# Optimization experiments

Measured on AMD Instinct MI355X. Metric: run time of the kernel, lower is better.

## Reference

```python
import jax, jax.numpy as jnp
import numpy as np
from jax import lax

EPS = 1e-5
MIN_SAMPLES = 4
RESHAPE = 14        # edge-map downsample factor
KEEP_FRAC = 0.1     # 1 - quantile(0.9)
KERNEL_FRAC = 0.05  # eval-mode log_kernel

SOBEL_X = jnp.array([[-1., 0., 1.], [-2., 0., 2.], [-1., 0., 1.]], jnp.float32)
SOBEL_Y = jnp.array([[-1., -2., -1.], [0., 0., 0.], [1., 2., 1.]], jnp.float32)


def _dwconv3(x, k):
    C = x.shape[1]
    kern = jnp.broadcast_to(k, (C, 1, 3, 3)).astype(x.dtype)
    return lax.conv_general_dilated(x, kern, (1, 1), 'SAME',
        feature_group_count=C, dimension_numbers=('NCHW', 'OIHW', 'NCHW'))


def _erode3(m):
    k = jnp.ones((1, 1, 3, 3), m.dtype)
    s = lax.conv_general_dilated(m, k, (1, 1), 'SAME',
        dimension_numbers=('NCHW', 'OIHW', 'NCHW'))
    return (s >= 9.0).astype(m.dtype)


def _masked_mean(x, mask, axis=-1):
    m = mask.astype(x.dtype)
    return jnp.sum(x * m, axis=axis) / jnp.maximum(jnp.sum(m, axis=axis), 1.0)


def _ssi_norm(x, mask):
    # scale-shift-invariant normalization: masked median shift, masked MAD scale
    big = jnp.where(mask, x, jnp.inf)
    srt = jnp.sort(big, axis=-1)
    n = jnp.sum(mask, axis=-1)
    idx = jnp.maximum((n - 1) // 2, 0)
    med = jnp.take_along_axis(srt, idx[..., None], axis=-1)
    med = jnp.where(n[..., None] > 0, med, 0.0)
    scale = _masked_mean(jnp.abs(x - med), mask, axis=-1)[..., None]
    return (x - med) / jnp.maximum(scale, EPS)


def _get_edge(image, vmask):
    gx = _dwconv3(image, SOBEL_X) / 8.0
    gy = _dwconv3(image, SOBEL_Y) / 8.0
    gx = jnp.sqrt(jnp.mean(gx * gx, axis=1, keepdims=True))
    gy = jnp.sqrt(jnp.mean(gy * gy, axis=1, keepdims=True))
    edges = jnp.sqrt(gx * gx + gy * gy)
    H, W = edges.shape[-2:]
    bm = jnp.zeros((H, W), edges.dtype).at[3:H - 3, 3:W - 3].set(1.0)
    return edges * bm * vmask


def _resize_bilinear(x, oh, ow):
    # torch F.interpolate bilinear, align_corners=False, no antialias
    B, C, H, W = x.shape
    def coords(o, s):
        c = jnp.clip((jnp.arange(o) + 0.5) * (s / o) - 0.5, 0.0, s - 1.0)
        i0 = jnp.floor(c).astype(jnp.int32)
        return i0, jnp.minimum(i0 + 1, s - 1), c - i0
    y0, y1, wy = coords(oh, H)
    x0, x1, wx = coords(ow, W)
    wy = wy[:, None]; wx = wx[None, :]
    g = lambda yi, xi: x[:, :, yi[:, None], xi[None, :]]
    return (g(y0, x0) * (1 - wy) * (1 - wx) + g(y0, x1) * (1 - wy) * wx
          + g(y1, x0) * wy * (1 - wx) + g(y1, x1) * wy * wx)


def _sample_edges(edges):
    B, _, H, W = edges.shape
    oh, ow = H // RESHAPE, W // RESHAPE
    e = _resize_bilinear(edges, oh, ow).reshape(B, -1)
    k = max(int(KEEP_FRAC * oh * ow), 10)
    _, idx = lax.top_k(e, k)
    return jnp.stack([(idx // ow) * RESHAPE, (idx % ow) * RESHAPE], -1).astype(jnp.int32)


def _extract_patches(x, coords, kh, kw):
    # vectorized irregular patch gather: [B,C,H,W] + [B,P,2] -> [B,P*C,kh*kw]
    B, C, H, W = x.shape
    ph, pw = kh // 2, kw // 2
    xp = jnp.pad(x, ((0, 0), (0, 0), (ph, ph), (pw, pw)))
    dy = jnp.arange(-ph, ph + 1)
    dx = jnp.arange(-pw, pw + 1)
    def one(img, y, x_):
        return img[:, (y + dy)[:, None], (x_ + dx)[None, :]]
    patches = jax.vmap(jax.vmap(one, in_axes=(None, 0, 0)))(
        xp, coords[..., 0] + ph, coords[..., 1] + pw)  # [B,P,C,kh,kw]
    return patches.reshape(B, -1, kh * kw)


def _forward(inp, tgt, mask, image, vmask):
    mask = mask.astype(bool)
    inp = inp.astype(jnp.float32)
    tgt = tgt.astype(jnp.float32)
    B, _, H, W = inp.shape
    vm = _erode3(vmask.astype(jnp.float32))
    edges = _get_edge(image.astype(jnp.float32), vm)
    coords = _sample_edges(edges)
    ks = int(KERNEL_FRAC * min(H, W))
    ks += int(ks % 2 == 0)
    # local patch branch
    pin = _extract_patches(inp, coords, ks, ks)
    ptg = _extract_patches(tgt, coords, ks, ks)
    pmk = _extract_patches(mask.astype(jnp.float32), coords, ks, ks) > 0.5
    pin = _ssi_norm(pin, pmk)
    ptg = _ssi_norm(ptg, pmk)
    err = jnp.maximum(jnp.abs(pin - ptg), EPS)
    valid = jnp.sum(pmk, axis=-1) >= MIN_SAMPLES
    ep = jnp.sqrt(jnp.maximum(_masked_mean(err, pmk, -1), EPS))  # [B,P]
    e_patch = _masked_mean(ep, valid, -1)                         # [B]
    # global image branch
    gi = _ssi_norm(inp.reshape(B, 1, H * W), mask.reshape(B, 1, H * W))
    gt = _ssi_norm(tgt.reshape(B, 1, H * W), mask.reshape(B, 1, H * W))
    gerr = jnp.maximum(jnp.abs(gi - gt), EPS)
    e_glob = jnp.sqrt(jnp.maximum(_masked_mean(gerr, mask.reshape(B, 1, H * W), -1), EPS)).squeeze(-1)
    return 0.5 * (e_patch + e_glob)  # [B]


def setup_inputs() -> dict:
    key = jax.random.key(0)
    k1, k2, k3, k4 = jax.random.split(key, 4)
    B, H, W = 32, 480, 640
    return {
        'input': jax.random.uniform(k1, (B, 1, H, W), jnp.float32, 0.1, 10.0),
        'target': jax.random.uniform(k2, (B, 1, H, W), jnp.float32, 0.1, 10.0),
        'mask': jax.random.bernoulli(k3, 0.9, (B, 1, H, W)),
        'image': jax.random.normal(k4, (B, 3, H, W), jnp.float32),
        'validity_mask': jnp.ones((B, 1, H, W), bool),
    }


def reference(input, target, mask, image, validity_mask):
    return _forward(input, target, mask, image, validity_mask)
```

## Files before the change

### kernel.cpp

```cpp
#include <hip/hip_runtime.h>
#include <math.h>

#define BB 32
#define HH 480
#define WW 640
#define HWN (HH * WW)
#define OH 34
#define OW 45
#define OHW (OH * OW)
#define KTOP 153
#define KS 25
#define PHW 12
#define PATCH (KS * KS)
#define RESHAPE_I 14
#define EPSV 1e-5f

#define TSLICE 10
#define TSW (OHW / TSLICE)

#define NB12 4096
#define PSLICE 32
#define NSLICE 16
#define CAP 32768
#define LCAP 2048
#define CPAD 32

__device__ __forceinline__ unsigned int fkey(float f) {
  unsigned int u = __float_as_uint(f);
  return (u & 0x80000000u) ? ~u : (u | 0x80000000u);
}
__device__ __forceinline__ float fkey_inv(unsigned int k) {
  unsigned int u = (k & 0x80000000u) ? (k & 0x7FFFFFFFu) : ~k;
  return __uint_as_float(u);
}

__device__ __forceinline__ float breduce256(float v, float* red) {
  const int t = threadIdx.x;
  __syncthreads();
  red[t] = v;
  __syncthreads();
  for (int s2 = 128; s2 > 0; s2 >>= 1) {
    if (t < s2) red[t] += red[t + s2];
    __syncthreads();
  }
  float r = red[0];
  __syncthreads();
  return r;
}

__device__ __forceinline__ float2 breduce256x2(float a, float b, float* red) {
  const int t = threadIdx.x;
  __syncthreads();
  red[t] = a;
  red[256 + t] = b;
  __syncthreads();
  for (int s2 = 128; s2 > 0; s2 >>= 1) {
    if (t < s2) {
      red[t] += red[t + s2];
      red[256 + t] += red[256 + t + s2];
    }
    __syncthreads();
  }
  float2 r = make_float2(red[0], red[256]);
  __syncthreads();
  return r;
}

__device__ float edge_at(const float* __restrict__ image, const unsigned char* __restrict__ vmask,
                         int b, int y, int x) {
  if (y < 3 || y >= HH - 3 || x < 3 || x >= WW - 3) return 0.f;
  const unsigned char* vm = vmask + (size_t)b * HWN;
  #pragma unroll
  for (int dy = -1; dy <= 1; ++dy) {
    #pragma unroll
    for (int dx = -1; dx <= 1; ++dx) {
      if (!vm[(size_t)(y + dy) * WW + (x + dx)]) return 0.f;
    }
  }
  const float* img = image + (size_t)b * 3 * HWN;
  float sx2 = 0.f, sy2 = 0.f;
  #pragma unroll
  for (int c = 0; c < 3; ++c) {
    const float* p = img + (size_t)c * HWN + (size_t)y * WW + x;
    float a00 = p[-WW - 1], a01 = p[-WW], a02 = p[-WW + 1];
    float a10 = p[-1],                    a12 = p[1];
    float a20 = p[WW - 1],  a21 = p[WW],  a22 = p[WW + 1];
    float gx = (-a00 + a02 + -2.f * a10 + 2.f * a12 + -a20 + a22) / 8.f;
    float gy = (-a00 + -2.f * a01 + -a02 + a20 + 2.f * a21 + a22) / 8.f;
    sx2 += gx * gx;
    sy2 += gy * gy;
  }
  float gxm = sqrtf(sx2 / 3.f);
  float gym = sqrtf(sy2 / 3.f);
  return sqrtf(gxm * gxm + gym * gym);
}

__global__ __launch_bounds__(256) void edge_resize_kernel(const float* __restrict__ image,
                                                          const unsigned char* __restrict__ vmask,
                                                          float* __restrict__ re) {
  int gid = blockIdx.x * 256 + threadIdx.x;
  int corner = gid & 3;
  int cell = gid >> 2;
  int b = cell / OHW;
  int rem = cell % OHW;
  int oy = rem / OW, ox = rem % OW;

  const float ry = (float)((double)HH / (double)OH);
  const float rx = (float)((double)WW / (double)OW);
  float cy = fminf(fmaxf(((float)oy + 0.5f) * ry - 0.5f, 0.f), (float)(HH - 1));
  float cx = fminf(fmaxf(((float)ox + 0.5f) * rx - 0.5f, 0.f), (float)(WW - 1));
  int y0 = (int)floorf(cy);
  int x0 = (int)floorf(cx);
  int y1 = min(y0 + 1, HH - 1);
  int x1 = min(x0 + 1, WW - 1);
  float wy = cy - (float)y0;
  float wx = cx - (float)x0;

  int yy = (corner & 2) ? y1 : y0;
  int xx = (corner & 1) ? x1 : x0;
  float w = ((corner & 2) ? wy : 1.f - wy) * ((corner & 1) ? wx : 1.f - wx);
  float g = edge_at(image, vmask, b, yy, xx) * w;
  g += __shfl_xor(g, 1, 64);
  g += __shfl_xor(g, 2, 64);
  if (corner == 0) re[cell] = g;
}

__global__ __launch_bounds__(256) void topk_rank_kernel(const float* __restrict__ re,
                                                        int* __restrict__ rpart) {
  const int b = blockIdx.x / TSLICE;
  const int sl = blockIdx.x % TSLICE;
  const int t = threadIdx.x;
  __shared__ float e[OHW];
  for (int i = t; i < OHW; i += 256) e[i] = re[b * OHW + i];
  __syncthreads();

  float vi[6];
  int idx[6], cnt[6];
  #pragma unroll
  for (int q = 0; q < 6; ++q) {
    int i = t + q * 256;
    idx[q] = i;
    vi[q] = (i < OHW) ? e[i] : 0.f;
    cnt[q] = 0;
  }
  const int j0 = sl * TSW;
  for (int jj = 0; jj < TSW; ++jj) {
    int j = j0 + jj;
    float u = e[j];
    #pragma unroll
    for (int q = 0; q < 6; ++q) {
      cnt[q] += (u > vi[q]) || (u == vi[q] && j < idx[q]);
    }
  }
  int* rp = rpart + ((size_t)b * TSLICE + sl) * OHW;
  #pragma unroll
  for (int q = 0; q < 6; ++q) {
    if (idx[q] < OHW) rp[idx[q]] = cnt[q];
  }
}

__global__ __launch_bounds__(256) void topk_write_kernel(const int* __restrict__ rpart,
                                                         int* __restrict__ coords) {
  const int b = blockIdx.x;
  const int t = threadIdx.x;
  const int* rp = rpart + (size_t)b * TSLICE * OHW;
  for (int i = t; i < OHW; i += 256) {
    int rank = 0;
    #pragma unroll
    for (int sl = 0; sl < TSLICE; ++sl) rank += rp[sl * OHW + i];
    if (rank < KTOP) {
      coords[(b * KTOP + rank) * 2 + 0] = (i / OW) * RESHAPE_I;
      coords[(b * KTOP + rank) * 2 + 1] = (i % OW) * RESHAPE_I;
    }
  }
}

__global__ __launch_bounds__(64) void patch_kernel(const float* __restrict__ inp,
                                                   const float* __restrict__ tgt,
                                                   const unsigned char* __restrict__ mask,
                                                   const int* __restrict__ coords,
                                                   float* __restrict__ ep, float* __restrict__ val) {
  const int bk = blockIdx.x;
  const int b = bk / KTOP;
  const int t = threadIdx.x;
  __shared__ unsigned int hist[512];
  __shared__ unsigned int sh_pref[2];
  __shared__ int sh_rank[2];

  const int cy = coords[bk * 2 + 0];
  const int cx = coords[bk * 2 + 1];

  float v_in[10], v_tg[10];
  unsigned int k_in[10], k_tg[10];
  unsigned int mbits = 0;
  #pragma unroll
  for (int q = 0; q < 10; ++q) {
    int i = t + q * 64;
    float vi = 0.f, vt = 0.f;
    if (i < PATCH) {
      int dy = i / KS - PHW, dx = i % KS - PHW;
      int y = cy + dy, x = cx + dx;
      if (y >= 0 && y < HH && x >= 0 && x < WW) {
        size_t off = (size_t)b * HWN + (size_t)y * WW + x;
        if (mask[off]) mbits |= (1u << q);
        vi = inp[off];
        vt = tgt[off];
      }
    }
    v_in[q] = vi; v_tg[q] = vt;
    k_in[q] = fkey(vi); k_tg[q] = fkey(vt);
  }

  int pn = __popc(mbits);
  #pragma unroll
  for (int d = 32; d > 0; d >>= 1) pn += __shfl_xor(pn, d, 64);
  const int n = pn;
  const float nf = (float)n;
  const int r = (n > 0) ? ((n - 1) >> 1) : 0;

  if (t == 0) {
    sh_pref[0] = 0; sh_pref[1] = 0;
    sh_rank[0] = r; sh_rank[1] = r;
  }
  __syncthreads();

  #pragma unroll
  for (int p = 0; p < 4; ++p) {
    const int shift = 24 - 8 * p;
    #pragma unroll
    for (int j = 0; j < 8; ++j) hist[t + 64 * j] = 0;
    __syncthreads();
    const int r_in = sh_rank[0], r_tg = sh_rank[1];
    const unsigned int pref_in = sh_pref[0], pref_tg = sh_pref[1];
    #pragma unroll
    for (int q = 0; q < 10; ++q) {
      if (mbits & (1u << q)) {
        unsigned int k = k_in[q];
        if (p == 0 || (k >> (shift + 8)) == pref_in)
          atomicAdd(&hist[(k >> shift) & 255u], 1u);
        unsigned int k2 = k_tg[q];
        if (p == 0 || (k2 >> (shift + 8)) == pref_tg)
          atomicAdd(&hist[256 + ((k2 >> shift) & 255u)], 1u);
      }
    }
    __syncthreads();
    {
      unsigned int a0 = hist[t * 4 + 0], a1 = hist[t * 4 + 1];
      unsigned int a2 = hist[t * 4 + 2], a3 = hist[t * 4 + 3];
      unsigned int b0 = hist[256 + t * 4 + 0], b1 = hist[256 + t * 4 + 1];
      unsigned int b2 = hist[256 + t * 4 + 2], b3 = hist[256 + t * 4 + 3];
      unsigned int sa0 = a0, sa1 = sa0 + a1, sa2 = sa1 + a2, sa3 = sa2 + a3;
      unsigned int sb0 = b0, sb1 = sb0 + b1, sb2 = sb1 + b2, sb3 = sb2 + b3;
      unsigned int ta = sa3, tb = sb3;
      #pragma unroll
      for (int d = 1; d < 64; d <<= 1) {
        unsigned int ua = (unsigned int)__shfl_up((int)ta, d, 64);
        unsigned int ub = (unsigned int)__shfl_up((int)tb, d, 64);
        if (t >= d) { ta += ua; tb += ub; }
      }
      unsigned int exa = ta - sa3, exb = tb - sb3;
      unsigned int rra = (unsigned int)r_in, rrb = (unsigned int)r_tg;
      unsigned int pa[4] = {exa, exa + sa0, exa + sa1, exa + sa2};
      unsigned int ca[4] = {exa + sa0, exa + sa1, exa + sa2, exa + sa3};
      unsigned int pb[4] = {exb, exb + sb0, exb + sb1, exb + sb2};
      unsigned int cb[4] = {exb + sb0, exb + sb1, exb + sb2, exb + sb3};
      #pragma unroll
      for (int j = 0; j < 4; ++j) {
        if (rra >= pa[j] && rra < ca[j]) {
          sh_pref[0] = (pref_in << 8) | (unsigned int)(t * 4 + j);
          sh_rank[0] = (int)(rra - pa[j]);
        }
        if (rrb >= pb[j] && rrb < cb[j]) {
          sh_pref[1] = (pref_tg << 8) | (unsigned int)(t * 4 + j);
          sh_rank[1] = (int)(rrb - pb[j]);
        }
      }
    }
    __syncthreads();
  }

  const float med_i = (n > 0) ? fkey_inv(sh_pref[0]) : 0.f;
  const float med_t = (n > 0) ? fkey_inv(sh_pref[1]) : 0.f;

  float pi = 0.f, pt = 0.f;
  #pragma unroll
  for (int q = 0; q < 10; ++q) {
    if (mbits & (1u << q)) {
      pi += fabsf(v_in[q] - med_i);
      pt += fabsf(v_tg[q] - med_t);
    }
  }
  #pragma unroll
  for (int d = 32; d > 0; d >>= 1) {
    pi += __shfl_xor(pi, d, 64);
    pt += __shfl_xor(pt, d, 64);
  }
  const float si = fmaxf(pi / fmaxf(nf, 1.f), EPSV);
  const float st = fmaxf(pt / fmaxf(nf, 1.f), EPSV);

  float pe = 0.f;
  #pragma unroll
  for (int q = 0; q < 10; ++q) {
    if (mbits & (1u << q)) {
      float a = (v_in[q] - med_i) / si;
      float c = (v_tg[q] - med_t) / st;
      pe += fmaxf(fabsf(a - c), EPSV);
    }
  }
  #pragma unroll
  for (int d = 32; d > 0; d >>= 1) pe += __shfl_xor(pe, d, 64);

  if (t == 0) {
    ep[bk] = sqrtf(fmaxf(pe / fmaxf(nf, 1.f), EPSV));
    val[bk] = (n >= 4) ? 1.f : 0.f;
  }
}

__global__ __launch_bounds__(256) void preduce_kernel(const float* __restrict__ ep,
                                                      const float* __restrict__ val,
                                                      float* __restrict__ e_patch) {
  const int b = blockIdx.x;
  const int t = threadIdx.x;
  __shared__ float red[512];
  float se = 0.f, sv = 0.f;
  for (int i = t; i < KTOP; i += 256) {
    float v = val[b * KTOP + i];
    se += ep[b * KTOP + i] * v;
    sv += v;
  }
  float2 tt = breduce256x2(se, sv, red);
  if (t == 0) e_patch[b] = tt.x / fmaxf(tt.y, 1.f);
}

__global__ __launch_bounds__(256) void gpass12_kernel(const float* __restrict__ inp,
                                                      const float* __restrict__ tgt,
                                                      const unsigned char* __restrict__ mask,
                                                      unsigned int* __restrict__ ghist) {
  const int b = blockIdx.x / PSLICE;
  const int sl = blockIdx.x % PSLICE;
  const int t = threadIdx.x;
  __shared__ unsigned int hist[2 * NB12];
  for (int i = t; i < 2 * NB12; i += 256) hist[i] = 0;
  __syncthreads();
  const float4* xi4 = (const float4*)(inp + (size_t)b * HWN);
  const float4* xt4 = (const float4*)(tgt + (size_t)b * HWN);
  const unsigned int* m4 = (const unsigned int*)(mask + (size_t)b * HWN);
  const int per4 = (HWN / PSLICE) / 4;
  const int s0 = sl * per4;
  for (int i = s0 + t; i < s0 + per4; i += 256) {
    unsigned int mm = m4[i];
    if (!mm) continue;
    float4 a = xi4[i], c = xt4[i];
    if (mm & 0x000000FFu) { atomicAdd(&hist[fkey(a.x) >> 20], 1u); atomicAdd(&hist[NB12 + (fkey(c.x) >> 20)], 1u); }
    if (mm & 0x0000FF00u) { atomicAdd(&hist[fkey(a.y) >> 20], 1u); atomicAdd(&hist[NB12 + (fkey(c.y) >> 20)], 1u); }
    if (mm & 0x00FF0000u) { atomicAdd(&hist[fkey(a.z) >> 20], 1u); atomicAdd(&hist[NB12 + (fkey(c.z) >> 20)], 1u); }
    if (mm & 0xFF000000u) { atomicAdd(&hist[fkey(a.w) >> 20], 1u); atomicAdd(&hist[NB12 + (fkey(c.w) >> 20)], 1u); }
  }
  __syncthreads();
  for (int i = t; i < NB12; i += 256) {
    unsigned int h0 = hist[i], h1 = hist[NB12 + i];
    if (h0) atomicAdd(&ghist[(size_t)(b * 2 + 0) * NB12 + i], h0);
    if (h1) atomicAdd(&ghist[(size_t)(b * 2 + 1) * NB12 + i], h1);
  }
}

__global__ __launch_bounds__(256) void gsel12_kernel(const unsigned int* __restrict__ ghist,
                                                     int* __restrict__ sel) {
  const int bs = blockIdx.x;
  const int t = threadIdx.x;
  const unsigned int* gh = ghist + (size_t)bs * NB12;
  __shared__ unsigned int scan[256];
  unsigned int local[16];
  unsigned int s = 0;
  const int base = t * 16;
  #pragma unroll
  for (int j = 0; j < 16; ++j) {
    local[j] = gh[base + j];
    s += local[j];
  }
  scan[t] = s;
  __syncthreads();
  for (int d = 1; d < 256; d <<= 1) {
    unsigned int v = (t >= d) ? scan[t - d] : 0u;
    __syncthreads();
    scan[t] += v;
    __syncthreads();
  }
  const unsigned int incl = scan[t];
  const unsigned int ex = incl - s;
  const unsigned int n = scan[255];
  if (n == 0) {
    if (t == 0) {
      sel[bs * 4 + 0] = -1;
      sel[bs * 4 + 1] = 0;
      sel[bs * 4 + 2] = 0;
      sel[bs * 4 + 3] = 0;
    }
    return;
  }
  const unsigned int r = (n - 1) >> 1;
  if (r >= ex && r < incl) {
    unsigned int cum = ex;
    int bin = base;
    #pragma unroll
    for (int j = 0; j < 16; ++j) {
      unsigned int h = local[j];
      if (cum + h > r) { bin = base + j; break; }
      cum += h;
    }
    sel[bs * 4 + 0] = bin;
    sel[bs * 4 + 1] = (int)(r - cum);
    sel[bs * 4 + 2] = (int)n;
    sel[bs * 4 + 3] = (int)cum;
  }
}

__global__ __launch_bounds__(256) void gcollect_kernel(const float* __restrict__ inp,
                                                       const float* __restrict__ tgt,
                                                       const unsigned char* __restrict__ mask,
                                                       const int* __restrict__ sel,
                                                       float* __restrict__ cand,
                                                       unsigned int* __restrict__ ccount,
                                                       float* __restrict__ sbelow,
                                                       float* __restrict__ sabove) {
  const int bs = blockIdx.x / NSLICE;
  const int sl = blockIdx.x % NSLICE;
  const int b = bs >> 1, s = bs & 1;
  const float* x = (s == 0 ? inp : tgt) + (size_t)b * HWN;
  const unsigned char* m = mask + (size_t)b * HWN;
  const int prefix = sel[bs * 4 + 0];
  __shared__ float red[512];
  __shared__ float buf[LCAP];
  __shared__ unsigned int lcnt, gbase;
  const int t = threadIdx.x;
  if (t == 0) lcnt = 0;
  __syncthreads();
  float sb = 0.f, sa = 0.f;
  if (prefix >= 0) {
    float* cd = cand + (size_t)bs * CAP;
    const float4* x4 = (const float4*)x;
    const unsigned int* m4 = (const unsigned int*)m;
    const int per4 = (HWN / NSLICE) / 4;
    const int s0 = sl * per4;
    for (int i = s0 + t; i < s0 + per4; i += 256) {
      unsigned int mm = m4[i];
      if (!mm) continue;
      float4 a = x4[i];
      #define GCOL(av, bit) \
        if (mm & bit) { \
          float v = av; \
          int pf = (int)(fkey(v) >> 20); \
          if (pf < prefix) sb += v; \
          else if (pf > prefix) sa += v; \
          else { \
            unsigned int pos = atomicAdd(&lcnt, 1u); \
            if (pos < LCAP) buf[pos] = v; \
            else { \
              unsigned int g = atomicAdd(&ccount[bs * CPAD], 1u); \
              if (g < CAP) cd[g] = v; \
            } \
          } \
        }
      GCOL(a.x, 0x000000FFu)
      GCOL(a.y, 0x0000FF00u)
      GCOL(a.z, 0x00FF0000u)
      GCOL(a.w, 0xFF000000u)
      #undef GCOL
    }
  }
  __syncthreads();
  if (prefix >= 0) {
    unsigned int c = min(lcnt, (unsigned int)LCAP);
    if (t == 0 && c > 0) gbase = atomicAdd(&ccount[bs * CPAD], c);
    __syncthreads();
    if (c > 0) {
      float* cd = cand + (size_t)bs * CAP;
      unsigned int base = gbase;
      for (unsigned int i = t; i < c; i += 256) {
        unsigned int pos = base + i;
        if (pos < CAP) cd[pos] = buf[i];
      }
    }
  }
  float2 ts = breduce256x2(sb, sa, red);
  if (t == 0) {
    atomicAdd(&sbelow[bs], ts.x);
    atomicAdd(&sabove[bs], ts.y);
  }
}

__global__ __launch_bounds__(256) void gfinal_kernel(const float* __restrict__ cand,
                                                     const unsigned int* __restrict__ ccount,
                                                     const int* __restrict__ sel,
                                                     const float* __restrict__ sbelow,
                                                     const float* __restrict__ sabove,
                                                     float* __restrict__ gstats,
                                                     float* __restrict__ nvals) {
  const int bs = blockIdx.x;
  const int t = threadIdx.x;
  const int prefix = sel[bs * 4 + 0];
  const int r2 = sel[bs * 4 + 1];
  const int n = sel[bs * 4 + 2];
  const int nbelow = sel[bs * 4 + 3];
  __shared__ unsigned int hist[256];
  __shared__ float red[256];
  __shared__ int sh_bin, sh_r;
  const float* cd = cand + (size_t)bs * CAP;
  int c = (int)min(ccount[bs * CPAD], (unsigned int)CAP);
  if (prefix < 0) {
    if (t == 0) {
      gstats[bs * 2 + 0] = 0.f;
      gstats[bs * 2 + 1] = 0.f;
      if ((bs & 1) == 0) nvals[bs >> 1] = 0.f;
    }
    return;
  }

  hist[t] = 0;
  __syncthreads();
  for (int i = t; i < c; i += 256)
    atomicAdd(&hist[(fkey(cd[i]) >> 12) & 255u], 1u);
  __syncthreads();
  if (t == 0) {
    unsigned int rr = (unsigned int)r2, cum = 0;
    int bin = 0;
    for (; bin < 256; ++bin) {
      unsigned int h = hist[bin];
      if (cum + h > rr) break;
      cum += h;
    }
    sh_bin = bin;
    sh_r = (int)(rr - cum);
  }
  __syncthreads();
  const int bin1 = sh_bin;
  const int r3 = sh_r;

  hist[t] = 0;
  __syncthreads();
  for (int i = t; i < c; i += 256) {
    unsigned int k = fkey(cd[i]);
    if (((k >> 12) & 255u) == (unsigned int)bin1)
      atomicAdd(&hist[(k >> 4) & 255u], 1u);
  }
  __syncthreads();
  if (t == 0) {
    unsigned int rr = (unsigned int)r3, cum = 0;
    int bin = 0;
    for (; bin < 256; ++bin) {
      unsigned int h = hist[bin];
      if (cum + h > rr) break;
      cum += h;
    }
    sh_bin = bin;
    sh_r = (int)(rr - cum);
  }
  __syncthreads();
  const int bin2 = sh_bin;
  const int r4 = sh_r;

  if (t < 16) hist[t] = 0;
  __syncthreads();
  {
    const unsigned int want = (((unsigned int)bin1 << 8) | (unsigned int)bin2);
    for (int i = t; i < c; i += 256) {
      unsigned int k = fkey(cd[i]);
      if (((k >> 4) & 0xFFFFu) == want)
        atomicAdd(&hist[k & 15u], 1u);
    }
  }
  __syncthreads();
  __shared__ float sh_med;
  if (t == 0) {
    unsigned int rr = (unsigned int)r4, cum = 0;
    int bin = 0;
    for (; bin < 16; ++bin) {
      unsigned int h = hist[bin];
      if (cum + h > rr) break;
      cum += h;
    }
    unsigned int key = ((unsigned int)prefix << 20) |
                       ((unsigned int)bin1 << 12) |
                       ((unsigned int)bin2 << 4) | (unsigned int)bin;
    sh_med = fkey_inv(key);
  }
  __syncthreads();
  const float med = sh_med;

  float ps = 0.f;
  for (int i = t; i < c; i += 256) ps += fabsf(cd[i] - med);
  float scand = breduce256(ps, red);
  if (t == 0) {
    float nb = (float)nbelow;
    float na = (float)(n - nbelow - c);
    float num = (nb * med - sbelow[bs]) + (sabove[bs] - na * med) + scand;
    gstats[bs * 2 + 0] = med;
    gstats[bs * 2 + 1] = num / fmaxf((float)n, 1.f);
    if ((bs & 1) == 0) nvals[bs >> 1] = (float)n;
  }
}

__global__ __launch_bounds__(256) void gerr_kernel(const float* __restrict__ inp,
                                                   const float* __restrict__ tgt,
                                                   const unsigned char* __restrict__ mask,
                                                   const float* __restrict__ gstats,
                                                   float* __restrict__ gacc) {
  const int b = blockIdx.x / PSLICE;
  const int sl = blockIdx.x % PSLICE;
  __shared__ float red[256];
  const int t = threadIdx.x;
  const float med_i = gstats[(b * 2 + 0) * 2 + 0];
  const float sc_i = fmaxf(gstats[(b * 2 + 0) * 2 + 1], EPSV);
  const float med_t = gstats[(b * 2 + 1) * 2 + 0];
  const float sc_t = fmaxf(gstats[(b * 2 + 1) * 2 + 1], EPSV);
  const float ri = 1.f / sc_i, rt = 1.f / sc_t;
  const float4* xi4 = (const float4*)(inp + (size_t)b * HWN);
  const float4* xt4 = (const float4*)(tgt + (size_t)b * HWN);
  const unsigned int* m4 = (const unsigned int*)(mask + (size_t)b * HWN);
  const int per4 = (HWN / PSLICE) / 4;
  const int s0 = sl * per4;
  float part = 0.f;
  for (int i = s0 + t; i < s0 + per4; i += 256) {
    unsigned int mm = m4[i];
    if (!mm) continue;
    float4 a = xi4[i], c = xt4[i];
    if (mm & 0x000000FFu) part += fmaxf(fabsf((a.x - med_i) * ri - (c.x - med_t) * rt), EPSV);
    if (mm & 0x0000FF00u) part += fmaxf(fabsf((a.y - med_i) * ri - (c.y - med_t) * rt), EPSV);
    if (mm & 0x00FF0000u) part += fmaxf(fabsf((a.z - med_i) * ri - (c.z - med_t) * rt), EPSV);
    if (mm & 0xFF000000u) part += fmaxf(fabsf((a.w - med_i) * ri - (c.w - med_t) * rt), EPSV);
  }
  float tp = breduce256(part, red);
  if (t == 0) atomicAdd(&gacc[b], tp);
}

__global__ __launch_bounds__(64) void final_kernel(const float* __restrict__ gacc,
                                                   const float* __restrict__ nvals,
                                                   const float* __restrict__ e_patch,
                                                   float* __restrict__ out) {
  const int b = threadIdx.x;
  if (b < BB) {
    float n = nvals[b];
    float eg = sqrtf(fmaxf(gacc[b] / fmaxf(n, 1.f), EPSV));
    out[b] = 0.5f * (e_patch[b] + eg);
  }
}

extern "C" void kernel_launch(void* const* d_in, const int* in_sizes, int n_in,
                              void* d_out, int out_size, void* d_ws, size_t ws_size,
                              hipStream_t stream) {
  const float* inp = (const float*)d_in[0];
  const float* tgt = (const float*)d_in[1];
  const unsigned char* mask = (const unsigned char*)d_in[2];
  const float* image = (const float*)d_in[3];
  const unsigned char* vmask = (const unsigned char*)d_in[4];
  float* out = (float*)d_out;

  float* ws = (float*)d_ws;
  float* re = ws;
  int* coords = (int*)(ws + 48960);
  float* ep = ws + 48960 + 9792;
  float* val = ep + 4896;
  float* e_patch = val + 4896;
  float* gstats = e_patch + 32;
  float* nvals = gstats + 128;
  int* sel12 = (int*)(nvals + 32);
  float* cand = (float*)(sel12 + 256);
  unsigned int* ghist12 = (unsigned int*)(cand + (size_t)64 * CAP);
  unsigned int* ccount = ghist12 + (size_t)64 * NB12;
  float* sbelow = (float*)(ccount + 64 * CPAD);
  float* sabove = sbelow + 64;
  float* gacc = sabove + 64;
  size_t zero_bytes = ((size_t)64 * NB12 + 64 * CPAD + 64 + 64 + 32) * 4;
  hipMemsetAsync(ghist12, 0, zero_bytes, stream);

  int* rpart = (int*)cand;

  edge_resize_kernel<<<(BB * OHW * 4) / 256, 256, 0, stream>>>(image, vmask, re);
  topk_rank_kernel<<<BB * TSLICE, 256, 0, stream>>>(re, rpart);
  topk_write_kernel<<<BB, 256, 0, stream>>>(rpart, coords);
  patch_kernel<<<BB * KTOP, 64, 0, stream>>>(inp, tgt, mask, coords, ep, val);
  preduce_kernel<<<BB, 256, 0, stream>>>(ep, val, e_patch);
  gpass12_kernel<<<BB * PSLICE, 256, 0, stream>>>(inp, tgt, mask, ghist12);
  gsel12_kernel<<<BB * 2, 256, 0, stream>>>(ghist12, sel12);
  gcollect_kernel<<<BB * 2 * NSLICE, 256, 0, stream>>>(inp, tgt, mask, sel12, cand, ccount, sbelow, sabove);
  gfinal_kernel<<<BB * 2, 256, 0, stream>>>(cand, ccount, sel12, sbelow, sabove, gstats, nvals);
  gerr_kernel<<<BB * PSLICE, 256, 0, stream>>>(inp, tgt, mask, gstats, gacc);
  final_kernel<<<1, 64, 0, stream>>>(gacc, nvals, e_patch, out);
}
```

Baseline: 394.8 us.

## Merge independent pipeline stages into shared launches to cut kernel count

The global histogram pass and the edge/resize pass now run as block ranges of one launch. Likewise rank with median-bin select, collect with top-k write, and the patch loss with the global-median finalize each share a launch. The final reduction folds into the gerr kernel through a last-block atomic counter. Patch blocks appear to process four patches per 256-thread block and write per-batch numerator and denominator accumulators. The goal is to cut eleven launches to five and let independent work overlap on the GPU, at the cost of heterogeneous blocks and extra atomics and fences.

```diff
diff --git a/kernel.cpp b/kernel.cpp
--- a/kernel.cpp
+++ b/kernel.cpp
@@ -25,6 +25,9 @@
 #define LCAP 2048
 #define CPAD 32
 
+#define EDGE_BLKS ((BB * OHW * 4) / 256)
+#define PBLK (BB * KTOP / 4)
+
 __device__ __forceinline__ unsigned int fkey(float f) {
   unsigned int u = __float_as_uint(f);
   return (u & 0x80000000u) ? ~u : (u | 0x80000000u);
@@ -95,516 +98,527 @@
   return sqrtf(gxm * gxm + gym * gym);
 }
 
-__global__ __launch_bounds__(256) void edge_resize_kernel(const float* __restrict__ image,
-                                                          const unsigned char* __restrict__ vmask,
-                                                          float* __restrict__ re) {
-  int gid = blockIdx.x * 256 + threadIdx.x;
-  int corner = gid & 3;
-  int cell = gid >> 2;
-  int b = cell / OHW;
-  int rem = cell % OHW;
-  int oy = rem / OW, ox = rem % OW;
-
-  const float ry = (float)((double)HH / (double)OH);
-  const float rx = (float)((double)WW / (double)OW);
-  float cy = fminf(fmaxf(((float)oy + 0.5f) * ry - 0.5f, 0.f), (float)(HH - 1));
-  float cx = fminf(fmaxf(((float)ox + 0.5f) * rx - 0.5f, 0.f), (float)(WW - 1));
-  int y0 = (int)floorf(cy);
-  int x0 = (int)floorf(cx);
-  int y1 = min(y0 + 1, HH - 1);
-  int x1 = min(x0 + 1, WW - 1);
-  float wy = cy - (float)y0;
-  float wx = cx - (float)x0;
-
-  int yy = (corner & 2) ? y1 : y0;
-  int xx = (corner & 1) ? x1 : x0;
-  float w = ((corner & 2) ? wy : 1.f - wy) * ((corner & 1) ? wx : 1.f - wx);
-  float g = edge_at(image, vmask, b, yy, xx) * w;
-  g += __shfl_xor(g, 1, 64);
-  g += __shfl_xor(g, 2, 64);
-  if (corner == 0) re[cell] = g;
-}
-
-__global__ __launch_bounds__(256) void topk_rank_kernel(const float* __restrict__ re,
-                                                        int* __restrict__ rpart) {
-  const int b = blockIdx.x / TSLICE;
-  const int sl = blockIdx.x % TSLICE;
-  const int t = threadIdx.x;
-  __shared__ float e[OHW];
-  for (int i = t; i < OHW; i += 256) e[i] = re[b * OHW + i];
-  __syncthreads();
-
-  float vi[6];
-  int idx[6], cnt[6];
-  #pragma unroll
-  for (int q = 0; q < 6; ++q) {
-    int i = t + q * 256;
-    idx[q] = i;
-    vi[q] = (i < OHW) ? e[i] : 0.f;
-    cnt[q] = 0;
-  }
-  const int j0 = sl * TSW;
-  for (int jj = 0; jj < TSW; ++jj) {
-    int j = j0 + jj;
-    float u = e[j];
-    #pragma unroll
-    for (int q = 0; q < 6; ++q) {
-      cnt[q] += (u > vi[q]) || (u == vi[q] && j < idx[q]);
-    }
-  }
-  int* rp = rpart + ((size_t)b * TSLICE + sl) * OHW;
-  #pragma unroll
-  for (int q = 0; q < 6; ++q) {
-    if (idx[q] < OHW) rp[idx[q]] = cnt[q];
-  }
-}
-
-__global__ __launch_bounds__(256) void topk_write_kernel(const int* __restrict__ rpart,
-                                                         int* __restrict__ coords) {
-  const int b = blockIdx.x;
-  const int t = threadIdx.x;
-  const int* rp = rpart + (size_t)b * TSLICE * OHW;
-  for (int i = t; i < OHW; i += 256) {
-    int rank = 0;
-    #pragma unroll
-    for (int sl = 0; sl < TSLICE; ++sl) rank += rp[sl * OHW + i];
-    if (rank < KTOP) {
-      coords[(b * KTOP + rank) * 2 + 0] = (i / OW) * RESHAPE_I;
-      coords[(b * KTOP + rank) * 2 + 1] = (i % OW) * RESHAPE_I;
-    }
-  }
-}
-
-__global__ __launch_bounds__(64) void patch_kernel(const float* __restrict__ inp,
+__global__ __launch_bounds__(256) void k_hist_edge(const float* __restrict__ inp,
                                                    const float* __restrict__ tgt,
                                                    const unsigned char* __restrict__ mask,
-                                                   const int* __restrict__ coords,
-                                                   float* __restrict__ ep, float* __restrict__ val) {
-  const int bk = blockIdx.x;
-  const int b = bk / KTOP;
+                                                   const float* __restrict__ image,
+                                                   const unsigned char* __restrict__ vmask,
+                                                   float* __restrict__ re,
+                                                   unsigned int* __restrict__ ghist) {
+  __shared__ unsigned int hist[2 * NB12];
   const int t = threadIdx.x;
-  __shared__ unsigned int hist[512];
-  __shared__ unsigned int sh_pref[2];
-  __shared__ int sh_rank[2];
-
-  const int cy = coords[bk * 2 + 0];
-  const int cx = coords[bk * 2 + 1];
-
-  float v_in[10], v_tg[10];
-  unsigned int k_in[10], k_tg[10];
-  unsigned int mbits = 0;
-  #pragma unroll
-  for (int q = 0; q < 10; ++q) {
-    int i = t + q * 64;
-    float vi = 0.f, vt = 0.f;
-    if (i < PATCH) {
-      int dy = i / KS - PHW, dx = i % KS - PHW;
-      int y = cy + dy, x = cx + dx;
-      if (y >= 0 && y < HH && x >= 0 && x < WW) {
-        size_t off = (size_t)b * HWN + (size_t)y * WW + x;
-        if (mask[off]) mbits |= (1u << q);
-        vi = inp[off];
-        vt = tgt[off];
-      }
-    }
-    v_in[q] = vi; v_tg[q] = vt;
-    k_in[q] = fkey(vi); k_tg[q] = fkey(vt);
-  }
-
-  int pn = __popc(mbits);
-  #pragma unroll
-  for (int d = 32; d > 0; d >>= 1) pn += __shfl_xor(pn, d, 64);
-  const int n = pn;
-  const float nf = (float)n;
-  const int r = (n > 0) ? ((n - 1) >> 1) : 0;
-
-  if (t == 0) {
-    sh_pref[0] = 0; sh_pref[1] = 0;
-    sh_rank[0] = r; sh_rank[1] = r;
-  }
-  __syncthreads();
-
-  #pragma unroll
-  for (int p = 0; p < 4; ++p) {
-    const int shift = 24 - 8 * p;
-    #pragma unroll
-    for (int j = 0; j < 8; ++j) hist[t + 64 * j] = 0;
-    __syncthreads();
-    const int r_in = sh_rank[0], r_tg = sh_rank[1];
-    const unsigned int pref_in = sh_pref[0], pref_tg = sh_pref[1];
-    #pragma unroll
-    for (int q = 0; q < 10; ++q) {
-      if (mbits & (1u << q)) {
-        unsigned int k = k_in[q];
-        if (p == 0 || (k >> (shift + 8)) == pref_in)
-          atomicAdd(&hist[(k >> shift) & 255u], 1u);
-        unsigned int k2 = k_tg[q];
-        if (p == 0 || (k2 >> (shift + 8)) == pref_tg)
-          atomicAdd(&hist[256 + ((k2 >> shift) & 255u)], 1u);
-      }
-    }
-    __syncthreads();
-    {
-      unsigned int a0 = hist[t * 4 + 0], a1 = hist[t * 4 + 1];
-      unsigned int a2 = hist[t * 4 + 2], a3 = hist[t * 4 + 3];
-      unsigned int b0 = hist[256 + t * 4 + 0], b1 = hist[256 + t * 4 + 1];
-      unsigned int b2 = hist[256 + t * 4 + 2], b3 = hist[256 + t * 4 + 3];
-      unsigned int sa0 = a0, sa1 = sa0 + a1, sa2 = sa1 + a2, sa3 = sa2 + a3;
-      unsigned int sb0 = b0, sb1 = sb0 + b1, sb2 = sb1 + b2, sb3 = sb2 + b3;
-      unsigned int ta = sa3, tb = sb3;
+  if (blockIdx.x < BB * PSLICE) {
+    const int b = blockIdx.x / PSLICE;
+    const int sl = blockIdx.x % PSLICE;
+    for (int i = t; i < 2 * NB12; i += 256) hist[i] = 0;
+    __syncthreads();
+    const float4* xi4 = (const float4*)(inp + (size_t)b * HWN);
+    const float4* xt4 = (const float4*)(tgt + (size_t)b * HWN);
+    const unsigned int* m4 = (const unsigned int*)(mask + (size_t)b * HWN);
+    const int per4 = (HWN / PSLICE) / 4;
+    const int s0 = sl * per4;
+    for (int i = s0 + t; i < s0 + per4; i += 256) {
+      unsigned int mm = m4[i];
+      if (!mm) continue;
+      float4 a = xi4[i], c = xt4[i];
+      if (mm & 0x000000FFu) { atomicAdd(&hist[fkey(a.x) >> 20], 1u); atomicAdd(&hist[NB12 + (fkey(c.x) >> 20)], 1u); }
+      if (mm & 0x0000FF00u) { atomicAdd(&hist[fkey(a.y) >> 20], 1u); atomicAdd(&hist[NB12 + (fkey(c.y) >> 20)], 1u); }
+      if (mm & 0x00FF0000u) { atomicAdd(&hist[fkey(a.z) >> 20], 1u); atomicAdd(&hist[NB12 + (fkey(c.z) >> 20)], 1u); }
+      if (mm & 0xFF000000u) { atomicAdd(&hist[fkey(a.w) >> 20], 1u); atomicAdd(&hist[NB12 + (fkey(c.w) >> 20)], 1u); }
+    }
+    __syncthreads();
+    for (int i = t; i < NB12; i += 256) {
+      unsigned int h0 = hist[i], h1 = hist[NB12 + i];
+      if (h0) atomicAdd(&ghist[(size_t)(b * 2 + 0) * NB12 + i], h0);
+      if (h1) atomicAdd(&ghist[(size_t)(b * 2 + 1) * NB12 + i], h1);
+    }
+  } else {
+    int gid = (blockIdx.x - BB * PSLICE) * 256 + t;
+    int corner = gid & 3;
+    int cell = gid >> 2;
+    int b = cell / OHW;
+    int rem = cell % OHW;
+    int oy = rem / OW, ox = rem % OW;
+
+    const float ry = (float)((double)HH / (double)OH);
+    const float rx = (float)((double)WW / (double)OW);
+    float cy = fminf(fmaxf(((float)oy + 0.5f) * ry - 0.5f, 0.f), (float)(HH - 1));
+    float cx = fminf(fmaxf(((float)ox + 0.5f) * rx - 0.5f, 0.f), (float)(WW - 1));
+    int y0 = (int)floorf(cy);
+    int x0 = (int)floorf(cx);
+    int y1 = min(y0 + 1, HH - 1);
+    int x1 = min(x0 + 1, WW - 1);
+    float wy = cy - (float)y0;
+    float wx = cx - (float)x0;
+
+    int yy = (corner & 2) ? y1 : y0;
+    int xx = (corner & 1) ? x1 : x0;
+    float w = ((corner & 2) ? wy : 1.f - wy) * ((corner & 1) ? wx : 1.f - wx);
+    float g = edge_at(image, vmask, b, yy, xx) * w;
+    g += __shfl_xor(g, 1, 64);
+    g += __shfl_xor(g, 2, 64);
+    if (corner == 0) re[cell] = g;
+  }
+}
+
+__global__ __launch_bounds__(256) void k_rank_sel(const float* __restrict__ re,
+                                                  const unsigned int* __restrict__ ghist,
+                                                  int* __restrict__ rpart,
+                                                  int* __restrict__ sel) {
+  __shared__ float e[OHW];
+  __shared__ unsigned int scan[256];
+  const int t = threadIdx.x;
+  if (blockIdx.x < BB * TSLICE) {
+    const int b = blockIdx.x / TSLICE;
+    const int sl = blockIdx.x % TSLICE;
+    for (int i = t; i < OHW; i += 256) e[i] = re[b * OHW + i];
+    __syncthreads();
+
+    float vi[6];
+    int idx[6], cnt[6];
+    #pragma unroll
+    for (int q = 0; q < 6; ++q) {
+      int i = t + q * 256;
+      idx[q] = i;
+      vi[q] = (i < OHW) ? e[i] : 0.f;
+      cnt[q] = 0;
+    }
+    const int j0 = sl * TSW;
+    for (int jj = 0; jj < TSW; ++jj) {
+      int j = j0 + jj;
+      float u = e[j];
       #pragma unroll
-      for (int d = 1; d < 64; d <<= 1) {
-        unsigned int ua = (unsigned int)__shfl_up((int)ta, d, 64);
-        unsigned int ub = (unsigned int)__shfl_up((int)tb, d, 64);
-        if (t >= d) { ta += ua; tb += ub; }
-      }
-      unsigned int exa = ta - sa3, exb = tb - sb3;
-      unsigned int rra = (unsigned int)r_in, rrb = (unsigned int)r_tg;
-      unsigned int pa[4] = {exa, exa + sa0, exa + sa1, exa + sa2};
-      unsigned int ca[4] = {exa + sa0, exa + sa1, exa + sa2, exa + sa3};
-      unsigned int pb[4] = {exb, exb + sb0, exb + sb1, exb + sb2};
-      unsigned int cb[4] = {exb + sb0, exb + sb1, exb + sb2, exb + sb3};
+      for (int q = 0; q < 6; ++q) {
+        cnt[q] += (u > vi[q]) || (u == vi[q] && j < idx[q]);
+      }
+    }
+    int* rp = rpart + ((size_t)b * TSLICE + sl) * OHW;
+    #pragma unroll
+    for (int q = 0; q < 6; ++q) {
+      if (idx[q] < OHW) rp[idx[q]] = cnt[q];
+    }
+  } else {
+    const int bs = blockIdx.x - BB * TSLICE;
+    const unsigned int* gh = ghist + (size_t)bs * NB12;
+    unsigned int local[16];
+    unsigned int s = 0;
+    const int base = t * 16;
+    #pragma unroll
+    for (int j = 0; j < 16; ++j) {
+      local[j] = gh[base + j];
+      s += local[j];
+    }
+    scan[t] = s;
+    __syncthreads();
+    for (int d = 1; d < 256; d <<= 1) {
+      unsigned int v = (t >= d) ? scan[t - d] : 0u;
+      __syncthreads();
+      scan[t] += v;
+      __syncthreads();
+    }
+    const unsigned int incl = scan[t];
+    const unsigned int ex = incl - s;
+    const unsigned int n = scan[255];
+    if (n == 0) {
+      if (t == 0) {
+        sel[bs * 4 + 0] = -1;
+        sel[bs * 4 + 1] = 0;
+        sel[bs * 4 + 2] = 0;
+        sel[bs * 4 + 3] = 0;
+      }
+      return;
+    }
+    const unsigned int r = (n - 1) >> 1;
+    if (r >= ex && r < incl) {
+      unsigned int cum = ex;
+      int bin = base;
       #pragma unroll
-      for (int j = 0; j < 4; ++j) {
-        if (rra >= pa[j] && rra < ca[j]) {
-          sh_pref[0] = (pref_in << 8) | (unsigned int)(t * 4 + j);
-          sh_rank[0] = (int)(rra - pa[j]);
-        }
-        if (rrb >= pb[j] && rrb < cb[j]) {
-          sh_pref[1] = (pref_tg << 8) | (unsigned int)(t * 4 + j);
-          sh_rank[1] = (int)(rrb - pb[j]);
-        }
-      }
-    }
-    __syncthreads();
-  }
-
-  const float med_i = (n > 0) ? fkey_inv(sh_pref[0]) : 0.f;
-  const float med_t = (n > 0) ? fkey_inv(sh_pref[1]) : 0.f;
-
-  float pi = 0.f, pt = 0.f;
-  #pragma unroll
-  for (int q = 0; q < 10; ++q) {
-    if (mbits & (1u << q)) {
-      pi += fabsf(v_in[q] - med_i);
-      pt += fabsf(v_tg[q] - med_t);
-    }
-  }
-  #pragma unroll
-  for (int d = 32; d > 0; d >>= 1) {
-    pi += __shfl_xor(pi, d, 64);
-    pt += __shfl_xor(pt, d, 64);
-  }
-  const float si = fmaxf(pi / fmaxf(nf, 1.f), EPSV);
-  const float st = fmaxf(pt / fmaxf(nf, 1.f), EPSV);
-
-  float pe = 0.f;
-  #pragma unroll
-  for (int q = 0; q < 10; ++q) {
-    if (mbits & (1u << q)) {
-      float a = (v_in[q] - med_i) / si;
-      float c = (v_tg[q] - med_t) / st;
-      pe += fmaxf(fabsf(a - c), EPSV);
-    }
-  }
-  #pragma unroll
-  for (int d = 32; d > 0; d >>= 1) pe += __shfl_xor(pe, d, 64);
-
-  if (t == 0) {
-    ep[bk] = sqrtf(fmaxf(pe / fmaxf(nf, 1.f), EPSV));
-    val[bk] = (n >= 4) ? 1.f : 0.f;
-  }
-}
-
-__global__ __launch_bounds__(256) void preduce_kernel(const float* __restrict__ ep,
-                                                      const float* __restrict__ val,
-                                                      float* __restrict__ e_patch) {
-  const int b = blockIdx.x;
-  const int t = threadIdx.x;
-  __shared__ float red[512];
-  float se = 0.f, sv = 0.f;
-  for (int i = t; i < KTOP; i += 256) {
-    float v = val[b * KTOP + i];
-    se += ep[b * KTOP + i] * v;
-    sv += v;
-  }
-  float2 tt = breduce256x2(se, sv, red);
-  if (t == 0) e_patch[b] = tt.x / fmaxf(tt.y, 1.f);
-}
-
-__global__ __launch_bounds__(256) void gpass12_kernel(const float* __restrict__ inp,
-                                                      const float* __restrict__ tgt,
-                                                      const unsigned char* __restrict__ mask,
-                                                      unsigned int* __restrict__ ghist) {
-  const int b = blockIdx.x / PSLICE;
-  const int sl = blockIdx.x % PSLICE;
-  const int t = threadIdx.x;
-  __shared__ unsigned int hist[2 * NB12];
-  for (int i = t; i < 2 * NB12; i += 256) hist[i] = 0;
-  __syncthreads();
-  const float4* xi4 = (const float4*)(inp + (size_t)b * HWN);
-  const float4* xt4 = (const float4*)(tgt + (size_t)b * HWN);
-  const unsigned int* m4 = (const unsigned int*)(mask + (size_t)b * HWN);
-  const int per4 = (HWN / PSLICE) / 4;
-  const int s0 = sl * per4;
-  for (int i = s0 + t; i < s0 + per4; i += 256) {
-    unsigned int mm = m4[i];
-    if (!mm) continue;
-    float4 a = xi4[i], c = xt4[i];
-    if (mm & 0x000000FFu) { atomicAdd(&hist[fkey(a.x) >> 20], 1u); atomicAdd(&hist[NB12 + (fkey(c.x) >> 20)], 1u); }
-    if (mm & 0x0000FF00u) { atomicAdd(&hist[fkey(a.y) >> 20], 1u); atomicAdd(&hist[NB12 + (fkey(c.y) >> 20)], 1u); }
-    if (mm & 0x00FF0000u) { atomicAdd(&hist[fkey(a.z) >> 20], 1u); atomicAdd(&hist[NB12 + (fkey(c.z) >> 20)], 1u); }
-    if (mm & 0xFF000000u) { atomicAdd(&hist[fkey(a.w) >> 20], 1u); atomicAdd(&hist[NB12 + (fkey(c.w) >> 20)], 1u); }
-  }
-  __syncthreads();
-  for (int i = t; i < NB12; i += 256) {
-    unsigned int h0 = hist[i], h1 = hist[NB12 + i];
-    if (h0) atomicAdd(&ghist[(size_t)(b * 2 + 0) * NB12 + i], h0);
-    if (h1) atomicAdd(&ghist[(size_t)(b * 2 + 1) * NB12 + i], h1);
-  }
-}
-
-__global__ __launch_bounds__(256) void gsel12_kernel(const unsigned int* __restrict__ ghist,
-                                                     int* __restrict__ sel) {
-  const int bs = blockIdx.x;
-  const int t = threadIdx.x;
-  const unsigned int* gh = ghist + (size_t)bs * NB12;
-  __shared__ unsigned int scan[256];
-  unsigned int local[16];
-  unsigned int s = 0;
-  const int base = t * 16;
-  #pragma unroll
-  for (int j = 0; j < 16; ++j) {
-    local[j] = gh[base + j];
-    s += local[j];
-  }
-  scan[t] = s;
-  __syncthreads();
-  for (int d = 1; d < 256; d <<= 1) {
-    unsigned int v = (t >= d) ? scan[t - d] : 0u;
-    __syncthreads();
-    scan[t] += v;
-    __syncthreads();
-  }
-  const unsigned int incl = scan[t];
-  const unsigned int ex = incl - s;
-  const unsigned int n = scan[255];
-  if (n == 0) {
-    if (t == 0) {
-      sel[bs * 4 + 0] = -1;
-      sel[bs * 4 + 1] = 0;
-      sel[bs * 4 + 2] = 0;
-      sel[bs * 4 + 3] = 0;
-    }
-    return;
-  }
-  const unsigned int r = (n - 1) >> 1;
-  if (r >= ex && r < incl) {
-    unsigned int cum = ex;
-    int bin = base;
-    #pragma unroll
-    for (int j = 0; j < 16; ++j) {
-      unsigned int h = local[j];
-      if (cum + h > r) { bin = base + j; break; }
-      cum += h;
-    }
-    sel[bs * 4 + 0] = bin;
-    sel[bs * 4 + 1] = (int)(r - cum);
-    sel[bs * 4 + 2] = (int)n;
-    sel[bs * 4 + 3] = (int)cum;
-  }
-}
-
-__global__ __launch_bounds__(256) void gcollect_kernel(const float* __restrict__ inp,
+      for (int j = 0; j < 16; ++j) {
+        unsigned int h = local[j];
+        if (cum + h > r) { bin = base + j; break; }
+        cum += h;
+      }
+      sel[bs * 4 + 0] = bin;
+      sel[bs * 4 + 1] = (int)(r - cum);
+      sel[bs * 4 + 2] = (int)n;
+      sel[bs * 4 + 3] = (int)cum;
+    }
+  }
+}
+
+__global__ __launch_bounds__(256) void k_collect_write(const float* __restrict__ inp,
                                                        const float* __restrict__ tgt,
                                                        const unsigned char* __restrict__ mask,
                                                        const int* __restrict__ sel,
+                                                       const int* __restrict__ rpart,
                                                        float* __restrict__ cand,
                                                        unsigned int* __restrict__ ccount,
                                                        float* __restrict__ sbelow,
-                                                       float* __restrict__ sabove) {
-  const int bs = blockIdx.x / NSLICE;
-  const int sl = blockIdx.x % NSLICE;
-  const int b = bs >> 1, s = bs & 1;
-  const float* x = (s == 0 ? inp : tgt) + (size_t)b * HWN;
-  const unsigned char* m = mask + (size_t)b * HWN;
-  const int prefix = sel[bs * 4 + 0];
+                                                       float* __restrict__ sabove,
+                                                       int* __restrict__ coords) {
+  __shared__ float bufi[LCAP];
+  __shared__ float buft[LCAP];
   __shared__ float red[512];
-  __shared__ float buf[LCAP];
-  __shared__ unsigned int lcnt, gbase;
+  __shared__ unsigned int lcnti, lcntt, gbi, gbt;
   const int t = threadIdx.x;
-  if (t == 0) lcnt = 0;
-  __syncthreads();
-  float sb = 0.f, sa = 0.f;
-  if (prefix >= 0) {
-    float* cd = cand + (size_t)bs * CAP;
-    const float4* x4 = (const float4*)x;
-    const unsigned int* m4 = (const unsigned int*)m;
+  if (blockIdx.x < BB * NSLICE) {
+    const int b = blockIdx.x / NSLICE;
+    const int sl = blockIdx.x % NSLICE;
+    const int pi = sel[(b * 2 + 0) * 4];
+    const int pt = sel[(b * 2 + 1) * 4];
+    if (t == 0) { lcnti = 0; lcntt = 0; }
+    __syncthreads();
+    float sbi = 0.f, sai = 0.f, sbt = 0.f, sat = 0.f;
+    float* cdi = cand + (size_t)(b * 2 + 0) * CAP;
+    float* cdt = cand + (size_t)(b * 2 + 1) * CAP;
+    const float4* xi4 = (const float4*)(inp + (size_t)b * HWN);
+    const float4* xt4 = (const float4*)(tgt + (size_t)b * HWN);
+    const unsigned int* m4 = (const unsigned int*)(mask + (size_t)b * HWN);
     const int per4 = (HWN / NSLICE) / 4;
     const int s0 = sl * per4;
     for (int i = s0 + t; i < s0 + per4; i += 256) {
       unsigned int mm = m4[i];
       if (!mm) continue;
-      float4 a = x4[i];
-      #define GCOL(av, bit) \
+      float4 a = xi4[i], c = xt4[i];
+      #define GC2(av, cv, bit) \
         if (mm & bit) { \
           float v = av; \
           int pf = (int)(fkey(v) >> 20); \
-          if (pf < prefix) sb += v; \
-          else if (pf > prefix) sa += v; \
+          if (pf < pi) sbi += v; \
+          else if (pf > pi) sai += v; \
           else { \
-            unsigned int pos = atomicAdd(&lcnt, 1u); \
-            if (pos < LCAP) buf[pos] = v; \
-            else { \
-              unsigned int g = atomicAdd(&ccount[bs * CPAD], 1u); \
-              if (g < CAP) cd[g] = v; \
-            } \
+            unsigned int pos = atomicAdd(&lcnti, 1u); \
+            if (pos < LCAP) bufi[pos] = v; \
+            else { unsigned int g = atomicAdd(&ccount[(b * 2 + 0) * CPAD], 1u); if (g < CAP) cdi[g] = v; } \
+          } \
+          float w2 = cv; \
+          int pg = (int)(fkey(w2) >> 20); \
+          if (pg < pt) sbt += w2; \
+          else if (pg > pt) sat += w2; \
+          else { \
+            unsigned int pos = atomicAdd(&lcntt, 1u); \
+            if (pos < LCAP) buft[pos] = w2; \
+            else { unsigned int g = atomicAdd(&ccount[(b * 2 + 1) * CPAD], 1u); if (g < CAP) cdt[g] = w2; } \
           } \
         }
-      GCOL(a.x, 0x000000FFu)
-      GCOL(a.y, 0x0000FF00u)
-      GCOL(a.z, 0x00FF0000u)
-      GCOL(a.w, 0xFF000000u)
-      #undef GCOL
-    }
-  }
-  __syncthreads();
-  if (prefix >= 0) {
-    unsigned int c = min(lcnt, (unsigned int)LCAP);
-    if (t == 0 && c > 0) gbase = atomicAdd(&ccount[bs * CPAD], c);
-    __syncthreads();
-    if (c > 0) {
-      float* cd = cand + (size_t)bs * CAP;
-      unsigned int base = gbase;
-      for (unsigned int i = t; i < c; i += 256) {
-        unsigned int pos = base + i;
-        if (pos < CAP) cd[pos] = buf[i];
-      }
-    }
-  }
-  float2 ts = breduce256x2(sb, sa, red);
-  if (t == 0) {
-    atomicAdd(&sbelow[bs], ts.x);
-    atomicAdd(&sabove[bs], ts.y);
-  }
-}
-
-__global__ __launch_bounds__(256) void gfinal_kernel(const float* __restrict__ cand,
-                                                     const unsigned int* __restrict__ ccount,
-                                                     const int* __restrict__ sel,
-                                                     const float* __restrict__ sbelow,
-                                                     const float* __restrict__ sabove,
-                                                     float* __restrict__ gstats,
-                                                     float* __restrict__ nvals) {
-  const int bs = blockIdx.x;
-  const int t = threadIdx.x;
-  const int prefix = sel[bs * 4 + 0];
-  const int r2 = sel[bs * 4 + 1];
-  const int n = sel[bs * 4 + 2];
-  const int nbelow = sel[bs * 4 + 3];
-  __shared__ unsigned int hist[256];
+      GC2(a.x, c.x, 0x000000FFu)
+      GC2(a.y, c.y, 0x0000FF00u)
+      GC2(a.z, c.z, 0x00FF0000u)
+      GC2(a.w, c.w, 0xFF000000u)
+      #undef GC2
+    }
+    __syncthreads();
+    {
+      unsigned int ci = min(lcnti, (unsigned int)LCAP);
+      unsigned int ct = min(lcntt, (unsigned int)LCAP);
+      if (t == 0) {
+        if (ci > 0) gbi = atomicAdd(&ccount[(b * 2 + 0) * CPAD], ci);
+        if (ct > 0) gbt = atomicAdd(&ccount[(b * 2 + 1) * CPAD], ct);
+      }
+      __syncthreads();
+      for (unsigned int i = t; i < ci; i += 256) {
+        unsigned int pos = gbi + i;
+        if (pos < CAP) cdi[pos] = bufi[i];
+      }
+      for (unsigned int i = t; i < ct; i += 256) {
+        unsigned int pos = gbt + i;
+        if (pos < CAP) cdt[pos] = buft[i];
+      }
+    }
+    float2 r1 = breduce256x2(sbi, sai, red);
+    float2 r2 = breduce256x2(sbt, sat, red);
+    if (t == 0) {
+      atomicAdd(&sbelow[b * 2 + 0], r1.x);
+      atomicAdd(&sabove[b * 2 + 0], r1.y);
+      atomicAdd(&sbelow[b * 2 + 1], r2.x);
+      atomicAdd(&sabove[b * 2 + 1], r2.y);
+    }
+  } else {
+    const int b = blockIdx.x - BB * NSLICE;
+    const int* rp = rpart + (size_t)b * TSLICE * OHW;
+    for (int i = t; i < OHW; i += 256) {
+      int rank = 0;
+      #pragma unroll
+      for (int sl = 0; sl < TSLICE; ++sl) rank += rp[sl * OHW + i];
+      if (rank < KTOP) {
+        coords[(b * KTOP + rank) * 2 + 0] = (i / OW) * RESHAPE_I;
+        coords[(b * KTOP + rank) * 2 + 1] = (i % OW) * RESHAPE_I;
+      }
+    }
+  }
+}
+
+__global__ __launch_bounds__(256) void k_patch_gfinal(const float* __restrict__ inp,
+                                                      const float* __restrict__ tgt,
+                                                      const unsigned char* __restrict__ mask,
+                                                      const int* __restrict__ coords,
+                                                      const float* __restrict__ cand,
+                                                      const unsigned int* __restrict__ ccount,
+                                                      const int* __restrict__ sel,
+                                                      const float* __restrict__ sbelow,
+                                                      const float* __restrict__ sabove,
+                                                      float* __restrict__ gstats,
+                                                      float* __restrict__ nvals,
+                                                      float* __restrict__ epnum,
+                                                      float* __restrict__ epden) {
+  __shared__ unsigned int hist4[4][512];
+  __shared__ unsigned int pref4[4][2];
+  __shared__ int rank4[4][2];
+  __shared__ unsigned int ghisto[256];
   __shared__ float red[256];
   __shared__ int sh_bin, sh_r;
-  const float* cd = cand + (size_t)bs * CAP;
-  int c = (int)min(ccount[bs * CPAD], (unsigned int)CAP);
-  if (prefix < 0) {
+  __shared__ float sh_med;
+  const int tid = threadIdx.x;
+  if (blockIdx.x < PBLK) {
+    const int wid = tid >> 6;
+    const int t = tid & 63;
+    const int bk = blockIdx.x * 4 + wid;
+    const int b = bk / KTOP;
+    unsigned int* hist = hist4[wid];
+    unsigned int* sh_pref = pref4[wid];
+    int* sh_rank = rank4[wid];
+
+    const int cy = coords[bk * 2 + 0];
+    const int cx = coords[bk * 2 + 1];
+
+    float v_in[10], v_tg[10];
+    unsigned int k_in[10], k_tg[10];
+    unsigned int mbits = 0;
+    #pragma unroll
+    for (int q = 0; q < 10; ++q) {
+      int i = t + q * 64;
+      float vi = 0.f, vt = 0.f;
+      if (i < PATCH) {
+        int dy = i / KS - PHW, dx = i % KS - PHW;
+        int y = cy + dy, x = cx + dx;
+        if (y >= 0 && y < HH && x >= 0 && x < WW) {
+          size_t off = (size_t)b * HWN + (size_t)y * WW + x;
+          if (mask[off]) mbits |= (1u << q);
+          vi = inp[off];
+          vt = tgt[off];
+        }
+      }
+      v_in[q] = vi; v_tg[q] = vt;
+      k_in[q] = fkey(vi); k_tg[q] = fkey(vt);
+    }
+
+    int pn = __popc(mbits);
+    #pragma unroll
+    for (int d = 32; d > 0; d >>= 1) pn += __shfl_xor(pn, d, 64);
+    const int n = pn;
+    const float nf = (float)n;
+    const int r = (n > 0) ? ((n - 1) >> 1) : 0;
+
     if (t == 0) {
-      gstats[bs * 2 + 0] = 0.f;
-      gstats[bs * 2 + 1] = 0.f;
-      if ((bs & 1) == 0) nvals[bs >> 1] = 0.f;
-    }
-    return;
-  }
-
-  hist[t] = 0;
-  __syncthreads();
-  for (int i = t; i < c; i += 256)
-    atomicAdd(&hist[(fkey(cd[i]) >> 12) & 255u], 1u);
-  __syncthreads();
-  if (t == 0) {
-    unsigned int rr = (unsigned int)r2, cum = 0;
-    int bin = 0;
-    for (; bin < 256; ++bin) {
-      unsigned int h = hist[bin];
-      if (cum + h > rr) break;
-      cum += h;
-    }
-    sh_bin = bin;
-    sh_r = (int)(rr - cum);
-  }
-  __syncthreads();
-  const int bin1 = sh_bin;
-  const int r3 = sh_r;
-
-  hist[t] = 0;
-  __syncthreads();
-  for (int i = t; i < c; i += 256) {
-    unsigned int k = fkey(cd[i]);
-    if (((k >> 12) & 255u) == (unsigned int)bin1)
-      atomicAdd(&hist[(k >> 4) & 255u], 1u);
-  }
-  __syncthreads();
-  if (t == 0) {
-    unsigned int rr = (unsigned int)r3, cum = 0;
-    int bin = 0;
-    for (; bin < 256; ++bin) {
-      unsigned int h = hist[bin];
-      if (cum + h > rr) break;
-      cum += h;
-    }
-    sh_bin = bin;
-    sh_r = (int)(rr - cum);
-  }
-  __syncthreads();
-  const int bin2 = sh_bin;
-  const int r4 = sh_r;
-
-  if (t < 16) hist[t] = 0;
-  __syncthreads();
-  {
-    const unsigned int want = (((unsigned int)bin1 << 8) | (unsigned int)bin2);
+      sh_pref[0] = 0; sh_pref[1] = 0;
+      sh_rank[0] = r; sh_rank[1] = r;
+    }
+    __syncthreads();
+
+    #pragma unroll
+    for (int p = 0; p < 4; ++p) {
+      const int shift = 24 - 8 * p;
+      #pragma unroll
+      for (int j = 0; j < 8; ++j) hist[t + 64 * j] = 0;
+      __syncthreads();
+      const int r_in = sh_rank[0], r_tg = sh_rank[1];
+      const unsigned int pref_in = sh_pref[0], pref_tg = sh_pref[1];
+      #pragma unroll
+      for (int q = 0; q < 10; ++q) {
+        if (mbits & (1u << q)) {
+          unsigned int k = k_in[q];
+          if (p == 0 || (k >> (shift + 8)) == pref_in)
+            atomicAdd(&hist[(k >> shift) & 255u], 1u);
+          unsigned int k2 = k_tg[q];
+          if (p == 0 || (k2 >> (shift + 8)) == pref_tg)
+            atomicAdd(&hist[256 + ((k2 >> shift) & 255u)], 1u);
+        }
+      }
+      __syncthreads();
+      {
+        unsigned int a0 = hist[t * 4 + 0], a1 = hist[t * 4 + 1];
+        unsigned int a2 = hist[t * 4 + 2], a3 = hist[t * 4 + 3];
+        unsigned int b0 = hist[256 + t * 4 + 0], b1 = hist[256 + t * 4 + 1];
+        unsigned int b2 = hist[256 + t * 4 + 2], b3 = hist[256 + t * 4 + 3];
+        unsigned int sa0 = a0, sa1 = sa0 + a1, sa2 = sa1 + a2, sa3 = sa2 + a3;
+        unsigned int sb0 = b0, sb1 = sb0 + b1, sb2 = sb1 + b2, sb3 = sb2 + b3;
+        unsigned int ta = sa3, tb = sb3;
+        #pragma unroll
+        for (int d = 1; d < 64; d <<= 1) {
+          unsigned int ua = (unsigned int)__shfl_up((int)ta, d, 64);
+          unsigned int ub = (unsigned int)__shfl_up((int)tb, d, 64);
+          if (t >= d) { ta += ua; tb += ub; }
+        }
+        unsigned int exa = ta - sa3, exb = tb - sb3;
+        unsigned int rra = (unsigned int)r_in, rrb = (unsigned int)r_tg;
+        unsigned int pa[4] = {exa, exa + sa0, exa + sa1, exa + sa2};
+        unsigned int ca[4] = {exa + sa0, exa + sa1, exa + sa2, exa + sa3};
+        unsigned int pb[4] = {exb, exb + sb0, exb + sb1, exb + sb2};
+        unsigned int cb[4] = {exb + sb0, exb + sb1, exb + sb2, exb + sb3};
+        #pragma unroll
+        for (int j = 0; j < 4; ++j) {
+          if (rra >= pa[j] && rra < ca[j]) {
+            sh_pref[0] = (pref_in << 8) | (unsigned int)(t * 4 + j);
+            sh_rank[0] = (int)(rra - pa[j]);
+          }
+          if (rrb >= pb[j] && rrb < cb[j]) {
+            sh_pref[1] = (pref_tg << 8) | (unsigned int)(t * 4 + j);
+            sh_rank[1] = (int)(rrb - pb[j]);
+          }
+        }
+      }
+      __syncthreads();
+    }
+
+    const float med_i = (n > 0) ? fkey_inv(sh_pref[0]) : 0.f;
+    const float med_t = (n > 0) ? fkey_inv(sh_pref[1]) : 0.f;
+
+    float pi = 0.f, pt = 0.f;
+    #pragma unroll
+    for (int q = 0; q < 10; ++q) {
+      if (mbits & (1u << q)) {
+        pi += fabsf(v_in[q] - med_i);
+        pt += fabsf(v_tg[q] - med_t);
+      }
+    }
+    #pragma unroll
+    for (int d = 32; d > 0; d >>= 1) {
+      pi += __shfl_xor(pi, d, 64);
+      pt += __shfl_xor(pt, d, 64);
+    }
+    const float si = fmaxf(pi / fmaxf(nf, 1.f), EPSV);
+    const float st = fmaxf(pt / fmaxf(nf, 1.f), EPSV);
+
+    float pe = 0.f;
+    #pragma unroll
+    for (int q = 0; q < 10; ++q) {
+      if (mbits & (1u << q)) {
+        float a = (v_in[q] - med_i) / si;
+        float c = (v_tg[q] - med_t) / st;
+        pe += fmaxf(fabsf(a - c), EPSV);
+      }
+    }
+    #pragma unroll
+    for (int d = 32; d > 0; d >>= 1) pe += __shfl_xor(pe, d, 64);
+
+    if (t == 0) {
+      float valf = (n >= 4) ? 1.f : 0.f;
+      float epv = sqrtf(fmaxf(pe / fmaxf(nf, 1.f), EPSV));
+      atomicAdd(&epnum[b], epv * valf);
+      atomicAdd(&epden[b], valf);
+    }
+  } else {
+    const int bs = blockIdx.x - PBLK;
+    const int t = tid;
+    const int prefix = sel[bs * 4 + 0];
+    const int r2 = sel[bs * 4 + 1];
+    const int n = sel[bs * 4 + 2];
+    const int nbelow = sel[bs * 4 + 3];
+    const float* cd = cand + (size_t)bs * CAP;
+    int c = (int)min(ccount[bs * CPAD], (unsigned int)CAP);
+    if (prefix < 0) {
+      if (t == 0) {
+        gstats[bs * 2 + 0] = 0.f;
+        gstats[bs * 2 + 1] = 0.f;
+        if ((bs & 1) == 0) nvals[bs >> 1] = 0.f;
+      }
+      return;
+    }
+
+    ghisto[t] = 0;
+    __syncthreads();
+    for (int i = t; i < c; i += 256)
+      atomicAdd(&ghisto[(fkey(cd[i]) >> 12) & 255u], 1u);
+    __syncthreads();
+    if (t == 0) {
+      unsigned int rr = (unsigned int)r2, cum = 0;
+      int bin = 0;
+      for (; bin < 256; ++bin) {
+        unsigned int h = ghisto[bin];
+        if (cum + h > rr) break;
+        cum += h;
+      }
+      sh_bin = bin;
+      sh_r = (int)(rr - cum);
+    }
+    __syncthreads();
+    const int bin1 = sh_bin;
+    const int r3 = sh_r;
+
+    ghisto[t] = 0;
+    __syncthreads();
     for (int i = t; i < c; i += 256) {
       unsigned int k = fkey(cd[i]);
-      if (((k >> 4) & 0xFFFFu) == want)
-        atomicAdd(&hist[k & 15u], 1u);
-    }
-  }
-  __syncthreads();
-  __shared__ float sh_med;
-  if (t == 0) {
-    unsigned int rr = (unsigned int)r4, cum = 0;
-    int bin = 0;
-    for (; bin < 16; ++bin) {
-      unsigned int h = hist[bin];
-      if (cum + h > rr) break;
-      cum += h;
-    }
-    unsigned int key = ((unsigned int)prefix << 20) |
-                       ((unsigned int)bin1 << 12) |
-                       ((unsigned int)bin2 << 4) | (unsigned int)bin;
-    sh_med = fkey_inv(key);
-  }
-  __syncthreads();
-  const float med = sh_med;
-
-  float ps = 0.f;
-  for (int i = t; i < c; i += 256) ps += fabsf(cd[i] - med);
-  float scand = breduce256(ps, red);
-  if (t == 0) {
-    float nb = (float)nbelow;
-    float na = (float)(n - nbelow - c);
-    float num = (nb * med - sbelow[bs]) + (sabove[bs] - na * med) + scand;
-    gstats[bs * 2 + 0] = med;
-    gstats[bs * 2 + 1] = num / fmaxf((float)n, 1.f);
-    if ((bs & 1) == 0) nvals[bs >> 1] = (float)n;
-  }
-}
-
-__global__ __launch_bounds__(256) void gerr_kernel(const float* __restrict__ inp,
-                                                   const float* __restrict__ tgt,
-                                                   const unsigned char* __restrict__ mask,
-                                                   const float* __restrict__ gstats,
-                                                   float* __restrict__ gacc) {
+      if (((k >> 12) & 255u) == (unsigned int)bin1)
+        atomicAdd(&ghisto[(k >> 4) & 255u], 1u);
+    }
+    __syncthreads();
+    if (t == 0) {
+      unsigned int rr = (unsigned int)r3, cum = 0;
+      int bin = 0;
+      for (; bin < 256; ++bin) {
+        unsigned int h = ghisto[bin];
+        if (cum + h > rr) break;
+        cum += h;
+      }
+      sh_bin = bin;
+      sh_r = (int)(rr - cum);
+    }
+    __syncthreads();
+    const int bin2 = sh_bin;
+    const int r4 = sh_r;
+
+    if (t < 16) ghisto[t] = 0;
+    __syncthreads();
+    {
+      const unsigned int want = (((unsigned int)bin1 << 8) | (unsigned int)bin2);
+      for (int i = t; i < c; i += 256) {
+        unsigned int k = fkey(cd[i]);
+        if (((k >> 4) & 0xFFFFu) == want)
+          atomicAdd(&ghisto[k & 15u], 1u);
+      }
+    }
+    __syncthreads();
+    if (t == 0) {
+      unsigned int rr = (unsigned int)r4, cum = 0;
+      int bin = 0;
+      for (; bin < 16; ++bin) {
+        unsigned int h = ghisto[bin];
+        if (cum + h > rr) break;
+        cum += h;
+      }
+      unsigned int key = ((unsigned int)prefix << 20) |
+                         ((unsigned int)bin1 << 12) |
+                         ((unsigned int)bin2 << 4) | (unsigned int)bin;
+      sh_med = fkey_inv(key);
+    }
+    __syncthreads();
+    const float med = sh_med;
+
+    float ps = 0.f;
+    for (int i = t; i < c; i += 256) ps += fabsf(cd[i] - med);
+    float scand = breduce256(ps, red);
+    if (t == 0) {
+      float nb = (float)nbelow;
+      float na = (float)(n - nbelow - c);
+      float num = (nb * med - sbelow[bs]) + (sabove[bs] - na * med) + scand;
+      gstats[bs * 2 + 0] = med;
+      gstats[bs * 2 + 1] = num / fmaxf((float)n, 1.f);
+      if ((bs & 1) == 0) nvals[bs >> 1] = (float)n;
+    }
+  }
+}
+
+__global__ __launch_bounds__(256) void k_gerr_final(const float* __restrict__ inp,
+                                                    const float* __restrict__ tgt,
+                                                    const unsigned char* __restrict__ mask,
+                                                    const float* __restrict__ gstats,
+                                                    const float* __restrict__ nvals,
+                                                    const float* __restrict__ epnum,
+                                                    const float* __restrict__ epden,
+                                                    float* __restrict__ gacc,
+                                                    unsigned int* __restrict__ gdone,
+                                                    float* __restrict__ out) {
   const int b = blockIdx.x / PSLICE;
   const int sl = blockIdx.x % PSLICE;
   __shared__ float red[256];
@@ -630,18 +644,18 @@
     if (mm & 0xFF000000u) part += fmaxf(fabsf((a.w - med_i) * ri - (c.w - med_t) * rt), EPSV);
   }
   float tp = breduce256(part, red);
-  if (t == 0) atomicAdd(&gacc[b], tp);
-}
-
-__global__ __launch_bounds__(64) void final_kernel(const float* __restrict__ gacc,
-                                                   const float* __restrict__ nvals,
-                                                   const float* __restrict__ e_patch,
-                                                   float* __restrict__ out) {
-  const int b = threadIdx.x;
-  if (b < BB) {
-    float n = nvals[b];
-    float eg = sqrtf(fmaxf(gacc[b] / fmaxf(n, 1.f), EPSV));
-    out[b] = 0.5f * (e_patch[b] + eg);
+  if (t == 0) {
+    atomicAdd(&gacc[b], tp);
+    __threadfence();
+    unsigned int prev = atomicAdd(&gdone[b], 1u);
+    if (prev == PSLICE - 1) {
+      __threadfence();
+      float g = atomicAdd(&gacc[b], 0.0f);
+      float n = nvals[b];
+      float epb = epnum[b] / fmaxf(epden[b], 1.f);
+      float eg = sqrtf(fmaxf(g / fmaxf(n, 1.f), EPSV));
+      out[b] = 0.5f * (epb + eg);
+    }
   }
 }
 
@@ -658,32 +672,28 @@
   float* ws = (float*)d_ws;
   float* re = ws;
   int* coords = (int*)(ws + 48960);
-  float* ep = ws + 48960 + 9792;
-  float* val = ep + 4896;
-  float* e_patch = val + 4896;
-  float* gstats = e_patch + 32;
+  float* gstats = (float*)(coords + 9792);
   float* nvals = gstats + 128;
-  int* sel12 = (int*)(nvals + 32);
-  float* cand = (float*)(sel12 + 256);
-  unsigned int* ghist12 = (unsigned int*)(cand + (size_t)64 * CAP);
-  unsigned int* ccount = ghist12 + (size_t)64 * NB12;
+  int* sel = (int*)(nvals + 32);
+  int* rpart = sel + 256;
+  float* cand = (float*)(rpart + 489600);
+  unsigned int* ghist = (unsigned int*)(cand + (size_t)64 * CAP);
+  unsigned int* ccount = ghist + (size_t)64 * NB12;
   float* sbelow = (float*)(ccount + 64 * CPAD);
   float* sabove = sbelow + 64;
   float* gacc = sabove + 64;
-  size_t zero_bytes = ((size_t)64 * NB12 + 64 * CPAD + 64 + 64 + 32) * 4;
-  hipMemsetAsync(ghist12, 0, zero_bytes, stream);
-
-  int* rpart = (int*)cand;
-
-  edge_resize_kernel<<<(BB * OHW * 4) / 256, 256, 0, stream>>>(image, vmask, re);
-  topk_rank_kernel<<<BB * TSLICE, 256, 0, stream>>>(re, rpart);
-  topk_write_kernel<<<BB, 256, 0, stream>>>(rpart, coords);
-  patch_kernel<<<BB * KTOP, 64, 0, stream>>>(inp, tgt, mask, coords, ep, val);
-  preduce_kernel<<<BB, 256, 0, stream>>>(ep, val, e_patch);
-  gpass12_kernel<<<BB * PSLICE, 256, 0, stream>>>(inp, tgt, mask, ghist12);
-  gsel12_kernel<<<BB * 2, 256, 0, stream>>>(ghist12, sel12);
-  gcollect_kernel<<<BB * 2 * NSLICE, 256, 0, stream>>>(inp, tgt, mask, sel12, cand, ccount, sbelow, sabove);
-  gfinal_kernel<<<BB * 2, 256, 0, stream>>>(cand, ccount, sel12, sbelow, sabove, gstats, nvals);
-  gerr_kernel<<<BB * PSLICE, 256, 0, stream>>>(inp, tgt, mask, gstats, gacc);
-  final_kernel<<<1, 64, 0, stream>>>(gacc, nvals, e_patch, out);
-}
+  unsigned int* gdone = (unsigned int*)(gacc + 32);
+  float* epnum = (float*)(gdone + 32);
+  float* epden = epnum + 32;
+  size_t zero_bytes = ((size_t)64 * NB12 + 64 * CPAD + 64 + 64 + 32 + 32 + 32 + 32) * 4;
+  hipMemsetAsync(ghist, 0, zero_bytes, stream);
+
+  k_hist_edge<<<BB * PSLICE + EDGE_BLKS, 256, 0, stream>>>(inp, tgt, mask, image, vmask, re, ghist);
+  k_rank_sel<<<BB * TSLICE + 64, 256, 0, stream>>>(re, ghist, rpart, sel);
+  k_collect_write<<<BB * NSLICE + BB, 256, 0, stream>>>(inp, tgt, mask, sel, rpart, cand, ccount,
+                                                        sbelow, sabove, coords);
+  k_patch_gfinal<<<PBLK + 64, 256, 0, stream>>>(inp, tgt, mask, coords, cand, ccount, sel,
+                                                sbelow, sabove, gstats, nvals, epnum, epden);
+  k_gerr_final<<<BB * PSLICE, 256, 0, stream>>>(inp, tgt, mask, gstats, nvals, epnum, epden,
+                                                gacc, gdone, out);
+}
```

New measurement: 415.2 us. 5.2% more time.
